# Optimization experiments

Hardware: AMD Instinct MI355X
Metric: run time of the kernel (lower is better)

Reference implementation:

```python
import jax, jax.numpy as jnp
import numpy as np


def setup_inputs() -> dict:
    key = jax.random.key(0)
    ks = jax.random.split(key, 8)
    B, C, W, H = 4, 256, 64, 64
    Cq = C // 8
    return {
        "input": jax.random.normal(ks[0], (B, C, W, H), dtype=jnp.float32),
        "Wf": jax.random.normal(ks[1], (Cq, C), dtype=jnp.float32) * 0.05,
        "bf": jax.random.normal(ks[2], (Cq,), dtype=jnp.float32) * 0.05,
        "Wg": jax.random.normal(ks[3], (Cq, C), dtype=jnp.float32) * 0.05,
        "bg": jax.random.normal(ks[4], (Cq,), dtype=jnp.float32) * 0.05,
        "Wh": jax.random.normal(ks[5], (C, C), dtype=jnp.float32) * 0.05,
        "bh": jax.random.normal(ks[6], (C,), dtype=jnp.float32) * 0.05,
        "gamma": jax.random.normal(ks[7], (1,), dtype=jnp.float32),
    }


def reference(input, Wf, bf, Wg, bg, Wh, bh, gamma):
    # input: [B, C, W, H]; SAGAN self-attention over N = W*H spatial tokens.
    B, C, W, H = input.shape
    N = W * H
    x = input.reshape(B, C, N)
    # 1x1 Conv1d == per-token linear projection over channels.
    f = jnp.einsum('oc,bcn->bon', Wf, x) + bf[None, :, None]  # [B, C/8, N]
    g = jnp.einsum('oc,bcn->bon', Wg, x) + bg[None, :, None]  # [B, C/8, N]
    h = jnp.einsum('oc,bcn->bon', Wh, x) + bh[None, :, None]  # [B, C,   N]
    # s = f^T g -> [B, N, N]; softmax over last dim (columns / g-tokens).
    s = jnp.einsum('bon,bom->bnm', f, g)
    attention = jax.nn.softmax(s, axis=-1)
    # out = h @ attention^T : out[b,c,m] = sum_n h[b,c,n] * attention[b,m,n]
    out = jnp.einsum('bcn,bmn->bcm', h, attention)
    out = out.reshape(B, C, W, H)
    return gamma[0] * out + input
```

## Files before the change

kernel.cpp:

```cpp
#include <hip/hip_runtime.h>

typedef _Float16 half8 __attribute__((ext_vector_type(8)));
typedef _Float16 half4 __attribute__((ext_vector_type(4)));
typedef unsigned int uintx2 __attribute__((ext_vector_type(2)));
typedef unsigned int uintx4 __attribute__((ext_vector_type(4)));
typedef float floatx16 __attribute__((ext_vector_type(16)));

#define MFMA_F16(A, B, C) __builtin_amdgcn_mfma_f32_32x32x16_f16(A, B, C, 0, 0, 0)

constexpr int Bn = 4;
constexpr int Cc = 256;
constexpr int Cq = 32;
constexpr int Nn = 4096;
constexpr float LOG2E = 1.44269504088896340736f;


__device__ inline floatx16 zero16() {
  floatx16 z;
#pragma unroll
  for (int i = 0; i < 16; ++i) z[i] = 0.f;
  return z;
}

__device__ inline unsigned int pkrtz(float a, float b) {
  return __builtin_bit_cast(unsigned int, __builtin_amdgcn_cvt_pkrtz(a, b));
}

__global__ __launch_bounds__(256) void k_wconv(
    const float* __restrict__ Wf, const float* __restrict__ Wg,
    const float* __restrict__ Wh, _Float16* __restrict__ Wfh,
    _Float16* __restrict__ Wgh, _Float16* __restrict__ Whh) {
  int e = (blockIdx.x * 256 + threadIdx.x) * 4;
  const float* src;
  _Float16* dst;
  float sc = 1.f;
  if (e < 8192) { src = Wf + e; dst = Wfh + e; sc = LOG2E; }
  else if (e < 16384) { src = Wg + (e - 8192); dst = Wgh + (e - 8192); }
  else { src = Wh + (e - 16384); dst = Whh + (e - 16384); }
  float4 v = *(const float4*)src;
  half4 o;
  o[0] = (_Float16)(v.x * sc); o[1] = (_Float16)(v.y * sc);
  o[2] = (_Float16)(v.z * sc); o[3] = (_Float16)(v.w * sc);
  *(half4*)dst = o;
}

__global__ __launch_bounds__(256) void k_proj(
    const float* __restrict__ x,
    const _Float16* __restrict__ Wfh, const float* __restrict__ bf,
    const _Float16* __restrict__ Wgh, const float* __restrict__ bg,
    const _Float16* __restrict__ Whh, const float* __restrict__ bh,
    _Float16* __restrict__ Q, _Float16* __restrict__ K4,
    _Float16* __restrict__ V8) {
  __shared__ float xs[32][260];
  int tid = threadIdx.x;
  int w = tid >> 6, lane = tid & 63;
  int ml = lane & 31, h = lane >> 5;
  int b = blockIdx.x >> 7, nt = blockIdx.x & 127;
  int n0 = nt * 32;

  {
    int c = tid >> 3;
    int nl = (tid & 7) * 4;
    const float* xp = x + (size_t)b * Cc * Nn + n0 + nl;
#pragma unroll
    for (int pass = 0; pass < 8; ++pass) {
      int cc = c + pass * 32;
      float4 v = *(const float4*)(xp + (size_t)cc * Nn);
      xs[nl + 0][cc] = v.x;
      xs[nl + 1][cc] = v.y;
      xs[nl + 2][cc] = v.z;
      xs[nl + 3][cc] = v.w;
    }
  }
  __syncthreads();

  half8 bfr[16];
#pragma unroll
  for (int kc = 0; kc < 16; ++kc) {
    const float* xp = &xs[ml][kc * 16 + h * 8];
    half8 f;
#pragma unroll
    for (int j = 0; j < 8; ++j) f[j] = (_Float16)xp[j];
    bfr[kc] = f;
  }

  for (int t = w; t < 10; t += 4) {
    const _Float16* W;
    const float* bias;
    float bscale = 1.f;
    int o0 = 0;
    if (t == 0) { W = Wfh; bias = bf; bscale = LOG2E; }
    else if (t == 1) { W = Wgh; bias = bg; }
    else { W = Whh + (size_t)(t - 2) * 32 * Cc; bias = bh + (t - 2) * 32; o0 = (t - 2) * 32; }

    floatx16 acc = zero16();
    const _Float16* wp = W + (size_t)ml * Cc + h * 8;
#pragma unroll
    for (int kc = 0; kc < 16; ++kc) {
      half8 a = *(const half8*)(wp + kc * 16);
      acc = MFMA_F16(a, bfr[kc], acc);
    }

    if (t == 0) {
      _Float16* op = Q + ((size_t)b * Nn + n0 + ml) * Cq;
#pragma unroll
      for (int qd = 0; qd < 4; ++qd) {
        float4 bq = *(const float4*)(bias + 8 * qd + 4 * h);
        const float* bqp = (const float*)&bq;
#pragma unroll
        for (int i = 0; i < 4; ++i) {
          int crow = i + 8 * qd + 4 * h;
          op[crow] = (_Float16)(acc[4 * qd + i] + bqp[i] * bscale);
        }
      }
    } else if (t == 1) {
#pragma unroll
      for (int qd = 0; qd < 4; ++qd) {
        float4 bq = *(const float4*)(bias + 8 * qd + 4 * h);
        const float* bqp = (const float*)&bq;
#pragma unroll
        for (int i = 0; i < 4; ++i) {
          int crow = i + 8 * qd + 4 * h;
          K4[(((size_t)b * 4 + (crow >> 3)) * Nn + n0 + ml) * 8 + (crow & 7)] =
              (_Float16)(acc[4 * qd + i] + bqp[i]);
        }
      }
    } else {
      size_t nb = (size_t)((n0 + ml) >> 3);
      _Float16* op = V8 + (((size_t)b * 512 + nb) * 256) * 8 + (ml & 7);
#pragma unroll
      for (int qd = 0; qd < 4; ++qd) {
        float4 bq = *(const float4*)(bias + 8 * qd + 4 * h);
        const float* bqp = (const float*)&bq;
#pragma unroll
        for (int i = 0; i < 4; ++i) {
          int crow = i + 8 * qd + 4 * h;
          op[(size_t)(o0 + crow) * 8] = (_Float16)(acc[4 * qd + i] + bqp[i]);
        }
      }
    }
  }
}

__global__ __launch_bounds__(512) void k_rowmax(const _Float16* __restrict__ Q,
                                                const _Float16* __restrict__ K4,
                                                float* __restrict__ M) {
  __shared__ float red[8][32];
  int tid = threadIdx.x, w = tid >> 6, lane = tid & 63;
  int ml = lane & 31, h = lane >> 5;
  int b = blockIdx.x >> 7, mt = blockIdx.x & 127;
  int m0 = mt * 32;
  const _Float16* qp = Q + ((size_t)b * Nn + m0 + ml) * Cq + h * 8;
  half8 qb0 = *(const half8*)(qp);
  half8 qb1 = *(const half8*)(qp + 16);
  const _Float16* kp0 = K4 + (((size_t)b * 4 + h) * Nn + w * 512 + ml) * 8;
  const _Float16* kp1 = K4 + (((size_t)b * 4 + 2 + h) * Nn + w * 512 + ml) * 8;
  float mx = -3.0e38f;
  for (int t = 0; t < 16; ++t) {
    floatx16 s = zero16();
    half8 k0 = *(const half8*)(kp0 + (size_t)t * 32 * 8);
    half8 k1 = *(const half8*)(kp1 + (size_t)t * 32 * 8);
    s = MFMA_F16(k0, qb0, s);
    s = MFMA_F16(k1, qb1, s);
#pragma unroll
    for (int i = 0; i < 16; ++i) mx = fmaxf(mx, s[i]);
  }
  mx = fmaxf(mx, __shfl_xor(mx, 32, 64));
  if (h == 0) red[w][ml] = mx;
  __syncthreads();
  if (tid < 32) {
    float m2 = red[0][tid];
#pragma unroll
    for (int i = 1; i < 8; ++i) m2 = fmaxf(m2, red[i][tid]);
    M[(size_t)b * Nn + m0 + tid] = m2;
  }
}

__device__ inline void otree_write(float2* dst, const floatx16* o) {
#pragma unroll
  for (int cb = 0; cb < 8; ++cb)
#pragma unroll
    for (int rp = 0; rp < 8; ++rp)
      dst[(cb * 8 + rp) * 64] = make_float2(o[cb][2 * rp], o[cb][2 * rp + 1]);
}

__device__ inline void otree_add(const float2* src, floatx16* o) {
#pragma unroll
  for (int cb = 0; cb < 8; ++cb)
#pragma unroll
    for (int rp = 0; rp < 8; ++rp) {
      float2 v = src[(cb * 8 + rp) * 64];
      o[cb][2 * rp] += v.x;
      o[cb][2 * rp + 1] += v.y;
    }
}

__global__ __launch_bounds__(512, 2) void k_attn(
    const _Float16* __restrict__ Q, const _Float16* __restrict__ K4,
    const _Float16* __restrict__ V8, const float* __restrict__ M,
    const float* __restrict__ xin, const float* __restrict__ gamma,
    float* __restrict__ out) {
  __shared__ float Ored[4 * 8192];
  __shared__ float lred[8][32];
  int tid = threadIdx.x, w = tid >> 6, lane = tid & 63;
  int ml = lane & 31, h = lane >> 5;
  int bx = blockIdx.x;
  int mt = bx & 127, b = bx >> 7;
  int m0 = mt * 32;

  const _Float16* qp = Q + ((size_t)b * Nn + m0 + ml) * Cq + h * 8;
  half8 qb0 = *(const half8*)(qp);
  half8 qb1 = *(const half8*)(qp + 16);
  float Mv = M[(size_t)b * Nn + m0 + ml];
  float g = gamma[0];
  float lacc = 0.f;

  const _Float16* k4b0 = K4 + (((size_t)b * 4 + h) * Nn + w * 32 + ml) * 8;
  const _Float16* k4b1 = K4 + (((size_t)b * 4 + 2 + h) * Nn + w * 32 + ml) * 8;
  const _Float16* v8b = V8 + (((size_t)b * 512 + w * 4 + h) * 256 + ml) * 8;

  floatx16 o[8];
#pragma unroll
  for (int i = 0; i < 8; ++i) o[i] = zero16();

  half8 k0 = *(const half8*)(k4b0);
  half8 k1 = *(const half8*)(k4b1);

  for (int it = 0; it < 16; ++it) {
    floatx16 s = zero16();
    s = MFMA_F16(k0, qb0, s);
    s = MFMA_F16(k1, qb1, s);
    k0 = *(const half8*)(k4b0 + (size_t)(it + 1) * 2048);
    k1 = *(const half8*)(k4b1 + (size_t)(it + 1) * 2048);
    float p[16];
#pragma unroll
    for (int i = 0; i < 16; ++i) p[i] = __builtin_amdgcn_exp2f(s[i] - Mv);
#pragma unroll
    for (int i = 0; i < 16; ++i) lacc += p[i];
    unsigned int c0 = pkrtz(p[0], p[1]),  c1 = pkrtz(p[2], p[3]);
    unsigned int c2 = pkrtz(p[4], p[5]),  c3 = pkrtz(p[6], p[7]);
    unsigned int c4 = pkrtz(p[8], p[9]),  c5 = pkrtz(p[10], p[11]);
    unsigned int c6 = pkrtz(p[12], p[13]), c7 = pkrtz(p[14], p[15]);
    uintx2 t02 = __builtin_amdgcn_permlane32_swap(c0, c2, false, false);
    uintx2 t13 = __builtin_amdgcn_permlane32_swap(c1, c3, false, false);
    uintx2 t46 = __builtin_amdgcn_permlane32_swap(c4, c6, false, false);
    uintx2 t57 = __builtin_amdgcn_permlane32_swap(c5, c7, false, false);
    uintx4 f0v = {t02.x, t13.x, t02.y, t13.y};
    uintx4 f1v = {t46.x, t57.x, t46.y, t57.y};
    half8 pf0 = __builtin_bit_cast(half8, f0v);
    half8 pf1 = __builtin_bit_cast(half8, f1v);
    const _Float16* vp = v8b + (size_t)it * 65536;
#pragma unroll
    for (int cb = 0; cb < 8; ++cb) {
      half8 vf0 = *(const half8*)(vp + cb * 256);
      o[cb] = MFMA_F16(vf0, pf0, o[cb]);
    }
#pragma unroll
    for (int cb = 0; cb < 8; ++cb) {
      half8 vf1 = *(const half8*)(vp + 4096 + cb * 256);
      o[cb] = MFMA_F16(vf1, pf1, o[cb]);
    }
  }

  lacc += __shfl_xor(lacc, 32, 64);
  if (h == 0) lred[w][ml] = lacc;

  float2* Ored2 = (float2*)Ored;
  int lofs = h * 32 + ml;
  if (w >= 4) otree_write(Ored2 + (w - 4) * 4096 + lofs, o);
  __syncthreads();
  if (w < 4) otree_add(Ored2 + w * 4096 + lofs, o);
  __syncthreads();
  if (w == 2 || w == 3) otree_write(Ored2 + (w - 2) * 4096 + lofs, o);
  __syncthreads();
  if (w < 2) otree_add(Ored2 + w * 4096 + lofs, o);
  __syncthreads();
  if (w == 1) otree_write(Ored2 + lofs, o);
  __syncthreads();
  if (w == 0) { otree_add(Ored2 + lofs, o); otree_write(Ored2 + lofs, o); }
  __syncthreads();

  float lv = 0.f;
#pragma unroll
  for (int i = 0; i < 8; ++i) lv += lred[i][ml];
  float scale = g / lv;
  const float2* src = Ored2 + lofs;
  size_t obase = ((size_t)b * 256 + w * 32) * (size_t)Nn + m0 + ml;
#pragma unroll
  for (int rp = 0; rp < 8; ++rp) {
    float2 v = src[(w * 8 + rp) * 64];
    int r = 2 * rp;
    int cA = (r & 3) + 8 * (r >> 2) + 4 * h;
    size_t oa = obase + (size_t)cA * Nn;
    out[oa] = scale * v.x + xin[oa];
    out[oa + Nn] = scale * v.y + xin[oa + Nn];
  }
}

extern "C" void kernel_launch(void* const* d_in, const int* in_sizes, int n_in,
                              void* d_out, int out_size, void* d_ws,
                              size_t ws_size, hipStream_t stream) {
  const float* x = (const float*)d_in[0];
  const float* Wf = (const float*)d_in[1];
  const float* bf = (const float*)d_in[2];
  const float* Wg = (const float*)d_in[3];
  const float* bg = (const float*)d_in[4];
  const float* Wh = (const float*)d_in[5];
  const float* bh = (const float*)d_in[6];
  const float* gamma = (const float*)d_in[7];
  float* out = (float*)d_out;

  char* ws = (char*)d_ws;
  _Float16* Q  = (_Float16*)(ws);
  _Float16* K4 = (_Float16*)(ws + 1048576);
  _Float16* V8 = (_Float16*)(ws + 2097152);
  float*    M  = (float*)   (ws + 10485760);
  _Float16* Wfh = (_Float16*)(ws + 10551296);
  _Float16* Wgh = (_Float16*)(ws + 10567680);
  _Float16* Whh = (_Float16*)(ws + 10584064);

  k_wconv<<<dim3(80), dim3(256), 0, stream>>>(Wf, Wg, Wh, Wfh, Wgh, Whh);
  k_proj<<<dim3(512), dim3(256), 0, stream>>>(x, Wfh, bf, Wgh, bg, Whh, bh, Q, K4, V8);
  k_rowmax<<<dim3(512), dim3(512), 0, stream>>>(Q, K4, M);
  k_attn<<<dim3(512), dim3(512), 0, stream>>>(Q, K4, V8, M, x, gamma, out);
}
```

Measured before the change: 163.5 us.

## Fuse row-max pass into attention kernel and software-pipeline the QK scores

Measured after the change: 183.1 us. +12.0%, slower.

```diff
diff --git a/kernel.cpp b/kernel.cpp
--- a/kernel.cpp
+++ b/kernel.cpp
@@ -142,40 +142,6 @@
   }
 }
 
-__global__ __launch_bounds__(512) void k_rowmax(const _Float16* __restrict__ Q,
-                                                const _Float16* __restrict__ K4,
-                                                float* __restrict__ M) {
-  __shared__ float red[8][32];
-  int tid = threadIdx.x, w = tid >> 6, lane = tid & 63;
-  int ml = lane & 31, h = lane >> 5;
-  int b = blockIdx.x >> 7, mt = blockIdx.x & 127;
-  int m0 = mt * 32;
-  const _Float16* qp = Q + ((size_t)b * Nn + m0 + ml) * Cq + h * 8;
-  half8 qb0 = *(const half8*)(qp);
-  half8 qb1 = *(const half8*)(qp + 16);
-  const _Float16* kp0 = K4 + (((size_t)b * 4 + h) * Nn + w * 512 + ml) * 8;
-  const _Float16* kp1 = K4 + (((size_t)b * 4 + 2 + h) * Nn + w * 512 + ml) * 8;
-  float mx = -3.0e38f;
-  for (int t = 0; t < 16; ++t) {
-    floatx16 s = zero16();
-    half8 k0 = *(const half8*)(kp0 + (size_t)t * 32 * 8);
-    half8 k1 = *(const half8*)(kp1 + (size_t)t * 32 * 8);
-    s = MFMA_F16(k0, qb0, s);
-    s = MFMA_F16(k1, qb1, s);
-#pragma unroll
-    for (int i = 0; i < 16; ++i) mx = fmaxf(mx, s[i]);
-  }
-  mx = fmaxf(mx, __shfl_xor(mx, 32, 64));
-  if (h == 0) red[w][ml] = mx;
-  __syncthreads();
-  if (tid < 32) {
-    float m2 = red[0][tid];
-#pragma unroll
-    for (int i = 1; i < 8; ++i) m2 = fmaxf(m2, red[i][tid]);
-    M[(size_t)b * Nn + m0 + tid] = m2;
-  }
-}
-
 __device__ inline void otree_write(float2* dst, const floatx16* o) {
 #pragma unroll
   for (int cb = 0; cb < 8; ++cb)
@@ -197,11 +163,11 @@
 
 __global__ __launch_bounds__(512, 2) void k_attn(
     const _Float16* __restrict__ Q, const _Float16* __restrict__ K4,
-    const _Float16* __restrict__ V8, const float* __restrict__ M,
+    const _Float16* __restrict__ V8,
     const float* __restrict__ xin, const float* __restrict__ gamma,
     float* __restrict__ out) {
   __shared__ float Ored[4 * 8192];
-  __shared__ float lred[8][32];
+  __shared__ float red[8][32];
   int tid = threadIdx.x, w = tid >> 6, lane = tid & 63;
   int ml = lane & 31, h = lane >> 5;
   int bx = blockIdx.x;
@@ -211,27 +177,55 @@
   const _Float16* qp = Q + ((size_t)b * Nn + m0 + ml) * Cq + h * 8;
   half8 qb0 = *(const half8*)(qp);
   half8 qb1 = *(const half8*)(qp + 16);
-  float Mv = M[(size_t)b * Nn + m0 + ml];
   float g = gamma[0];
-  float lacc = 0.f;
 
   const _Float16* k4b0 = K4 + (((size_t)b * 4 + h) * Nn + w * 32 + ml) * 8;
   const _Float16* k4b1 = K4 + (((size_t)b * 4 + 2 + h) * Nn + w * 32 + ml) * 8;
   const _Float16* v8b = V8 + (((size_t)b * 512 + w * 4 + h) * 256 + ml) * 8;
 
+  float mx = -3.0e38f;
+  {
+    half8 a0 = *(const half8*)(k4b0);
+    half8 a1 = *(const half8*)(k4b1);
+    for (int it = 0; it < 16; ++it) {
+      floatx16 s = zero16();
+      s = MFMA_F16(a0, qb0, s);
+      s = MFMA_F16(a1, qb1, s);
+      a0 = *(const half8*)(k4b0 + (size_t)(it + 1) * 2048);
+      a1 = *(const half8*)(k4b1 + (size_t)(it + 1) * 2048);
+#pragma unroll
+      for (int i = 0; i < 16; ++i) mx = fmaxf(mx, s[i]);
+    }
+  }
+  mx = fmaxf(mx, __shfl_xor(mx, 32, 64));
+  if (h == 0) red[w][ml] = mx;
+  __syncthreads();
+  float Mv = red[0][ml];
+#pragma unroll
+  for (int i = 1; i < 8; ++i) Mv = fmaxf(Mv, red[i][ml]);
+  __syncthreads();
+
   floatx16 o[8];
 #pragma unroll
   for (int i = 0; i < 8; ++i) o[i] = zero16();
-
-  half8 k0 = *(const half8*)(k4b0);
-  half8 k1 = *(const half8*)(k4b1);
-
-  for (int it = 0; it < 16; ++it) {
-    floatx16 s = zero16();
+  float lacc = 0.f;
+
+  floatx16 s;
+  {
+    half8 k0 = *(const half8*)(k4b0);
+    half8 k1 = *(const half8*)(k4b1);
+    s = zero16();
     s = MFMA_F16(k0, qb0, s);
     s = MFMA_F16(k1, qb1, s);
-    k0 = *(const half8*)(k4b0 + (size_t)(it + 1) * 2048);
-    k1 = *(const half8*)(k4b1 + (size_t)(it + 1) * 2048);
+  }
+
+  for (int it = 0; it < 16; ++it) {
+    const _Float16* vp = v8b + (size_t)it * 65536;
+    half8 va[4];
+#pragma unroll
+    for (int cb = 0; cb < 4; ++cb) va[cb] = *(const half8*)(vp + cb * 256);
+    half8 kn0 = *(const half8*)(k4b0 + (size_t)(it + 1) * 2048);
+    half8 kn1 = *(const half8*)(k4b1 + (size_t)(it + 1) * 2048);
     float p[16];
 #pragma unroll
     for (int i = 0; i < 16; ++i) p[i] = __builtin_amdgcn_exp2f(s[i] - Mv);
@@ -249,21 +243,28 @@
     uintx4 f1v = {t46.x, t57.x, t46.y, t57.y};
     half8 pf0 = __builtin_bit_cast(half8, f0v);
     half8 pf1 = __builtin_bit_cast(half8, f1v);
-    const _Float16* vp = v8b + (size_t)it * 65536;
+    floatx16 sn = zero16();
+    sn = MFMA_F16(kn0, qb0, sn);
+    sn = MFMA_F16(kn1, qb1, sn);
+    __builtin_amdgcn_s_setprio(1);
+#pragma unroll
+    for (int cb = 0; cb < 4; ++cb) o[cb] = MFMA_F16(va[cb], pf0, o[cb]);
+#pragma unroll
+    for (int cb = 4; cb < 8; ++cb) {
+      half8 vf = *(const half8*)(vp + cb * 256);
+      o[cb] = MFMA_F16(vf, pf0, o[cb]);
+    }
 #pragma unroll
     for (int cb = 0; cb < 8; ++cb) {
-      half8 vf0 = *(const half8*)(vp + cb * 256);
-      o[cb] = MFMA_F16(vf0, pf0, o[cb]);
-    }
-#pragma unroll
-    for (int cb = 0; cb < 8; ++cb) {
-      half8 vf1 = *(const half8*)(vp + 4096 + cb * 256);
-      o[cb] = MFMA_F16(vf1, pf1, o[cb]);
-    }
+      half8 vf = *(const half8*)(vp + 4096 + cb * 256);
+      o[cb] = MFMA_F16(vf, pf1, o[cb]);
+    }
+    __builtin_amdgcn_s_setprio(0);
+    s = sn;
   }
 
   lacc += __shfl_xor(lacc, 32, 64);
-  if (h == 0) lred[w][ml] = lacc;
+  if (h == 0) red[w][ml] = lacc;
 
   float2* Ored2 = (float2*)Ored;
   int lofs = h * 32 + ml;
@@ -282,7 +283,7 @@
 
   float lv = 0.f;
 #pragma unroll
-  for (int i = 0; i < 8; ++i) lv += lred[i][ml];
+  for (int i = 0; i < 8; ++i) lv += red[i][ml];
   float scale = g / lv;
   const float2* src = Ored2 + lofs;
   size_t obase = ((size_t)b * 256 + w * 32) * (size_t)Nn + m0 + ml;
@@ -314,13 +315,11 @@
   _Float16* Q  = (_Float16*)(ws);
   _Float16* K4 = (_Float16*)(ws + 1048576);
   _Float16* V8 = (_Float16*)(ws + 2097152);
-  float*    M  = (float*)   (ws + 10485760);
   _Float16* Wfh = (_Float16*)(ws + 10551296);
   _Float16* Wgh = (_Float16*)(ws + 10567680);
   _Float16* Whh = (_Float16*)(ws + 10584064);
 
   k_wconv<<<dim3(80), dim3(256), 0, stream>>>(Wf, Wg, Wh, Wfh, Wgh, Whh);
   k_proj<<<dim3(512), dim3(256), 0, stream>>>(x, Wfh, bf, Wgh, bg, Whh, bh, Q, K4, V8);
-  k_rowmax<<<dim3(512), dim3(512), 0, stream>>>(Q, K4, M);
-  k_attn<<<dim3(512), dim3(512), 0, stream>>>(Q, K4, V8, M, x, gamma, out);
-}
+  k_attn<<<dim3(512), dim3(512), 0, stream>>>(Q, K4, V8, x, gamma, out);
+}
```
